# Kernel tuning notes

Hardware: AMD Instinct MI355X
Metric: run time of the kernel (lower is better)

The kernel has to match this reference:

```python
import jax, jax.numpy as jnp
import numpy as np

B, V, C, K = 8, 5000, 256, 200
LAMBDA_MIN, LAMBDA_MAX = 10.0, 1000.0


def get_mask(evals_x, evals_y, resolvant_gamma):
    # evals_[xy]: [B, K]
    scaling = jnp.maximum(jnp.max(evals_x, axis=1), jnp.max(evals_y, axis=1))[:, None]
    ex = (evals_x / scaling) ** resolvant_gamma  # [B, K]
    ey = (evals_y / scaling) ** resolvant_gamma  # [B, K]
    g1 = ex[:, :, None]  # [B, K, 1]
    g2 = ey[:, None, :]  # [B, 1, K]
    d1 = 1.0 / (g1 * g1 + 1.0)
    d2 = 1.0 / (g2 * g2 + 1.0)
    M_re = g2 * d2 - g1 * d1
    M_im = d2 - d1
    return M_re * M_re + M_im * M_im  # [B, K, K]


def setup_inputs() -> dict:
    key = jax.random.key(0)
    ks = jax.random.split(key, 6)
    feat_x = jax.random.normal(ks[0], (B, V, C), dtype=jnp.float32)
    feat_y = jax.random.normal(ks[1], (B, V, C), dtype=jnp.float32)
    # Laplacian-like nonnegative eigenvalues, bounded away from 0 so pow(., gamma) is smooth
    evals_x = jax.random.uniform(ks[2], (B, K), dtype=jnp.float32) * 10.0 + 0.01
    evals_y = jax.random.uniform(ks[3], (B, K), dtype=jnp.float32) * 10.0 + 0.01
    evecs_trans_x = jax.random.normal(ks[4], (B, K, V), dtype=jnp.float32) / np.sqrt(V)
    evecs_trans_y = jax.random.normal(ks[5], (B, K, V), dtype=jnp.float32) / np.sqrt(V)
    gamma_raw = jnp.asarray(0.0, dtype=jnp.float32)
    # softplus^{-1}(100) ~= 100 (log(exp(100)-1)); computed stably (exp(100) overflows fp32)
    lambda_raw = jnp.asarray(100.0, dtype=jnp.float32)
    return {
        "feat_x": feat_x, "feat_y": feat_y,
        "evals_x": evals_x, "evals_y": evals_y,
        "evecs_trans_x": evecs_trans_x, "evecs_trans_y": evecs_trans_y,
        "gamma_raw": gamma_raw, "lambda_raw": lambda_raw,
    }


def reference(feat_x, feat_y, evals_x, evals_y, evecs_trans_x, evecs_trans_y, gamma_raw, lambda_raw):
    # constrained parameters
    gamma = jax.nn.sigmoid(gamma_raw)
    lmbda = LAMBDA_MIN + jax.nn.softplus(lambda_raw) * (LAMBDA_MAX - LAMBDA_MIN) / LAMBDA_MAX
    lmbda = jnp.clip(lmbda, LAMBDA_MIN, LAMBDA_MAX)

    A = jnp.einsum('bkv,bvc->bkc', evecs_trans_x, feat_x)   # [B, K, C]
    Bc = jnp.einsum('bkv,bvc->bkc', evecs_trans_y, feat_y)  # [B, K, C]
    D = get_mask(evals_x, evals_y, gamma)                   # [B, K, K]

    A_A_t = jnp.einsum('bkc,blc->bkl', A, A)   # [B, K, K]
    B_A_t = jnp.einsum('bkc,blc->bkl', Bc, A)  # [B, K, K]

    # one batched solve for all (b, i): M[b,i] = A A^T + lmbda * diag(D[b,i,:])
    eye = jnp.eye(A_A_t.shape[-1], dtype=A_A_t.dtype)
    M = A_A_t[:, None, :, :] + lmbda * D[:, :, :, None] * eye  # [B, K, K, K]
    # Cxy[b, i, :] solves M[b,i] x = B_A_t[b, i, :]
    Cxy = jnp.linalg.solve(M, B_A_t[..., None])[..., 0]  # [B, K, K]
    return Cxy
```

## Files before the change

### kernel.cpp

```cpp
#include <hip/hip_runtime.h>
#include <math.h>

#define Bn 8
#define Vn 5000
#define Cn 256
#define Kn 200

#define AB_OFF  0
#define AAT_OFF 819200

__global__ __launch_bounds__(256) void k_gemm_ab(
    const float* __restrict__ fx, const float* __restrict__ fy,
    const float* __restrict__ etx, const float* __restrict__ ety,
    float* __restrict__ AB)
{
    __shared__ float Es[64 * 33];
    __shared__ float Fs[32 * 64];
    const int bid  = blockIdx.x;
    const int ks   = bid & 7;
    const int t    = bid >> 3;
    const int mat  = t >> 4;
    const int tile = t & 15;
    const int tr = tile >> 2, tc = tile & 3;
    const int b = mat & 7, which = mat >> 3;
    const float* __restrict__ E = (which ? ety : etx) + b * Kn * Vn;
    const float* __restrict__ F = (which ? fy : fx) + b * Vn * Cn;
    float* __restrict__ out = AB + mat * Kn * Cn;
    const int row0 = tr * 64, col0 = tc * 64;
    const int kstart = ks * 640;
    const int kend = (kstart + 640 < Vn) ? (kstart + 640) : Vn;
    const int tid = threadIdx.x;
    const int tx = tid & 15, ty = tid >> 4;
    float acc[4][4] = {};

    for (int k0 = kstart; k0 < kend; k0 += 32) {
#pragma unroll
        for (int i = 0; i < 8; ++i) {
            int idx = tid + i * 256;
            int r = idx >> 5, kk = idx & 31;
            int gr = row0 + r, gk = k0 + kk;
            Es[r * 33 + kk] = (gr < Kn && gk < kend) ? E[gr * Vn + gk] : 0.f;
        }
#pragma unroll
        for (int i = 0; i < 8; ++i) {
            int idx = tid + i * 256;
            int v = idx >> 6, cc = idx & 63;
            int gv = k0 + v;
            Fs[v * 64 + cc] = (gv < kend) ? F[gv * Cn + col0 + cc] : 0.f;
        }
        __syncthreads();
#pragma unroll
        for (int kk = 0; kk < 32; ++kk) {
            float a0 = Es[(ty * 4 + 0) * 33 + kk];
            float a1 = Es[(ty * 4 + 1) * 33 + kk];
            float a2 = Es[(ty * 4 + 2) * 33 + kk];
            float a3 = Es[(ty * 4 + 3) * 33 + kk];
            float4 bv = *(const float4*)&Fs[kk * 64 + tx * 4];
            acc[0][0] += a0 * bv.x; acc[0][1] += a0 * bv.y; acc[0][2] += a0 * bv.z; acc[0][3] += a0 * bv.w;
            acc[1][0] += a1 * bv.x; acc[1][1] += a1 * bv.y; acc[1][2] += a1 * bv.z; acc[1][3] += a1 * bv.w;
            acc[2][0] += a2 * bv.x; acc[2][1] += a2 * bv.y; acc[2][2] += a2 * bv.z; acc[2][3] += a2 * bv.w;
            acc[3][0] += a3 * bv.x; acc[3][1] += a3 * bv.y; acc[3][2] += a3 * bv.z; acc[3][3] += a3 * bv.w;
        }
        __syncthreads();
    }
#pragma unroll
    for (int m = 0; m < 4; ++m) {
        int gr = row0 + ty * 4 + m;
        if (gr < Kn) {
#pragma unroll
            for (int n = 0; n < 4; ++n)
                atomicAdd(&out[gr * Cn + col0 + tx * 4 + n], acc[m][n]);
        }
    }
}

__global__ __launch_bounds__(256) void k_gemm_nt(
    const float* __restrict__ AB, float* __restrict__ AAT)
{
    __shared__ float Xs[64 * 33];
    __shared__ float As[64 * 33];
    const int bid = blockIdx.x;
    const int mat = bid >> 4;
    const int tile = bid & 15;
    const int tr = tile >> 2, tc = tile & 3;
    const float* __restrict__ X  = AB + mat * Kn * Cn;
    const float* __restrict__ A2 = AB + (mat & 7) * Kn * Cn;
    float* __restrict__ out = AAT + mat * Kn * Kn;
    const int r0 = tr * 64, j0 = tc * 64;
    const int tid = threadIdx.x;
    const int tx = tid & 15, ty = tid >> 4;
    float acc[4][4] = {};

    for (int c0 = 0; c0 < Cn; c0 += 32) {
#pragma unroll
        for (int i = 0; i < 8; ++i) {
            int idx = tid + i * 256;
            int r = idx >> 5, kk = idx & 31;
            int gr = r0 + r;
            Xs[r * 33 + kk] = (gr < Kn) ? X[gr * Cn + c0 + kk] : 0.f;
            int gj = j0 + r;
            As[r * 33 + kk] = (gj < Kn) ? A2[gj * Cn + c0 + kk] : 0.f;
        }
        __syncthreads();
#pragma unroll
        for (int kk = 0; kk < 32; ++kk) {
            float a0 = Xs[(ty * 4 + 0) * 33 + kk];
            float a1 = Xs[(ty * 4 + 1) * 33 + kk];
            float a2 = Xs[(ty * 4 + 2) * 33 + kk];
            float a3 = Xs[(ty * 4 + 3) * 33 + kk];
            float b0 = As[(tx * 4 + 0) * 33 + kk];
            float b1 = As[(tx * 4 + 1) * 33 + kk];
            float b2 = As[(tx * 4 + 2) * 33 + kk];
            float b3 = As[(tx * 4 + 3) * 33 + kk];
            acc[0][0] += a0 * b0; acc[0][1] += a0 * b1; acc[0][2] += a0 * b2; acc[0][3] += a0 * b3;
            acc[1][0] += a1 * b0; acc[1][1] += a1 * b1; acc[1][2] += a1 * b2; acc[1][3] += a1 * b3;
            acc[2][0] += a2 * b0; acc[2][1] += a2 * b1; acc[2][2] += a2 * b2; acc[2][3] += a2 * b3;
            acc[3][0] += a3 * b0; acc[3][1] += a3 * b1; acc[3][2] += a3 * b2; acc[3][3] += a3 * b3;
        }
        __syncthreads();
    }
#pragma unroll
    for (int m = 0; m < 4; ++m) {
        int gr = r0 + ty * 4 + m;
        if (gr < Kn) {
#pragma unroll
            for (int n = 0; n < 4; ++n) {
                int gj = j0 + tx * 4 + n;
                if (gj < Kn) out[gr * Kn + gj] = acc[m][n];
            }
        }
    }
}

template<int QQ>
__device__ __forceinline__ void back_range(float y[4], const float* sM,
                                           const float* sInv, int lane,
                                           int khi, int klo)
{
    for (int k = khi; k >= klo; --k) {
        float xk = __shfl(y[QQ], k & 63) * sInv[k];
        if (lane == (k & 63)) y[QQ] = xk;
#pragma unroll
        for (int q2 = 0; q2 <= QQ; ++q2) {
            int r = lane + 64 * q2;
            if (r < k) y[q2] -= sM[r * 201 + k] * xk;
        }
    }
}

__global__ __launch_bounds__(512) void k_solve(
    const float* __restrict__ AAT,
    const float* __restrict__ evalx, const float* __restrict__ evaly,
    const float* __restrict__ graw, const float* __restrict__ lraw,
    float* __restrict__ out)
{
    __shared__ float sM[Kn * 201];
    __shared__ float sInv[Kn];
    __shared__ float sAux[8];
    const int bid = blockIdx.x;
    const int b = bid / 200;
    const int i = bid - b * 200;
    const int tid = threadIdx.x;
    const float* __restrict__ Sb = AAT + b * 40000;
    const float* __restrict__ Rb = AAT + 320000 + bid * 200;
    const float* __restrict__ ex = evalx + b * Kn;
    const float* __restrict__ ey = evaly + b * Kn;

    for (int e = tid; e < 40000; e += 512) {
        int r = e / 200;
        int c = e - r * 200;
        sM[r * 201 + c] = Sb[e];
    }
    if (tid < 200) sM[tid * 201 + 200] = Rb[tid];

    if (tid < 64) {
        float mx = 0.f;
        for (int j = tid; j < 200; j += 64) mx = fmaxf(mx, fmaxf(ex[j], ey[j]));
#pragma unroll
        for (int s = 32; s > 0; s >>= 1) mx = fmaxf(mx, __shfl_down(mx, s));
        if (tid == 0) sAux[0] = mx;
    }
    __syncthreads();

    if (tid < 200) {
        int r = tid;
        float s = sAux[0];
        float g = 1.f / (1.f + expf(-graw[0]));
        float lr = lraw[0];
        float sp = fmaxf(lr, 0.f) + log1pf(expf(-fabsf(lr)));
        float lmb = 10.f + sp * (990.f / 1000.f);
        lmb = fminf(fmaxf(lmb, 10.f), 1000.f);
        float gx = powf(ex[i] / s, g);
        float gy = powf(ey[r] / s, g);
        float d1 = 1.f / (gx * gx + 1.f);
        float d2 = 1.f / (gy * gy + 1.f);
        float re = gy * d2 - gx * d1;
        float im = d2 - d1;
        sM[r * 201 + r] += lmb * (re * re + im * im);
    }
    __syncthreads();

    const int w = tid >> 6, l = tid & 63;

    for (int k = 0; k < 200; k += 8) {
        if (tid < 64) {
            float p[4][8];
#pragma unroll
            for (int q = 0; q < 4; ++q) {
                int r = k + l + 64 * q;
                if (r < 200) {
#pragma unroll
                    for (int c = 0; c < 8; ++c) p[q][c] = sM[r * 201 + k + c];
                } else {
#pragma unroll
                    for (int c = 0; c < 8; ++c) p[q][c] = 0.f;
                }
            }
#pragma unroll
            for (int c = 0; c < 8; ++c) {
                float pivc = __shfl(p[0][c], c);
                float invp = 1.0f / pivc;
                float pr[8];
#pragma unroll
                for (int j = c + 1; j < 8; ++j) pr[j] = __shfl(p[0][j], c);
#pragma unroll
                for (int q = 0; q < 4; ++q) {
                    int r = k + l + 64 * q;
                    bool act = (r < 200) && (q > 0 || l > c);
                    if (act) {
                        float f = p[q][c] * invp;
                        p[q][c] = f;
#pragma unroll
                        for (int j = c + 1; j < 8; ++j) p[q][j] -= f * pr[j];
                    }
                }
            }
#pragma unroll
            for (int q = 0; q < 4; ++q) {
                int r = k + l + 64 * q;
                if (r < 200) {
#pragma unroll
                    for (int c = 0; c < 8; ++c) sM[r * 201 + k + c] = p[q][c];
                }
            }
        }
        __syncthreads();

        {
            int j = k + 8 + tid;
            if (j <= 200) {
                float u[8];
#pragma unroll
                for (int c = 0; c < 8; ++c) u[c] = sM[(k + c) * 201 + j];
#pragma unroll
                for (int c = 1; c < 8; ++c) {
                    float a = u[c];
#pragma unroll
                    for (int c2 = 0; c2 < c; ++c2)
                        a -= sM[(k + c) * 201 + k + c2] * u[c2];
                    u[c] = a;
                }
#pragma unroll
                for (int c = 0; c < 8; ++c) sM[(k + c) * 201 + j] = u[c];
            }
        }
        __syncthreads();

        {
            const int jb0 = k + 8;
            float pv[4][8];
#pragma unroll
            for (int ch = 0; ch < 4; ++ch) {
                int j = jb0 + ch * 64 + l;
                if (j <= 200) {
#pragma unroll
                    for (int c = 0; c < 8; ++c) pv[ch][c] = sM[(k + c) * 201 + j];
                }
            }
            for (int r = k + 8 + w; r < 200; r += 8) {
                float f[8];
#pragma unroll
                for (int c = 0; c < 8; ++c) f[c] = sM[r * 201 + k + c];
#pragma unroll
                for (int ch = 0; ch < 4; ++ch) {
                    int j = jb0 + ch * 64 + l;
                    if (j <= 200) {
                        float a = sM[r * 201 + j];
#pragma unroll
                        for (int c = 0; c < 8; ++c) a -= f[c] * pv[ch][c];
                        sM[r * 201 + j] = a;
                    }
                }
            }
        }
        __syncthreads();
    }

    if (tid < 200) sInv[tid] = 1.0f / sM[tid * 201 + tid];
    __syncthreads();

    if (tid < 64) {
        float y[4];
#pragma unroll
        for (int q = 0; q < 4; ++q) {
            int r = tid + 64 * q;
            y[q] = (r < 200) ? sM[r * 201 + 200] : 0.f;
        }
        back_range<3>(y, sM, sInv, tid, 199, 192);
        back_range<2>(y, sM, sInv, tid, 191, 128);
        back_range<1>(y, sM, sInv, tid, 127, 64);
        back_range<0>(y, sM, sInv, tid, 63, 0);
#pragma unroll
        for (int q = 0; q < 4; ++q) {
            int r = tid + 64 * q;
            if (r < 200) out[bid * 200 + r] = y[q];
        }
    }
}

extern "C" void kernel_launch(void* const* d_in, const int* in_sizes, int n_in,
                              void* d_out, int out_size, void* d_ws, size_t ws_size,
                              hipStream_t stream)
{
    const float* fx   = (const float*)d_in[0];
    const float* fy   = (const float*)d_in[1];
    const float* evx  = (const float*)d_in[2];
    const float* evy  = (const float*)d_in[3];
    const float* etx  = (const float*)d_in[4];
    const float* ety  = (const float*)d_in[5];
    const float* graw = (const float*)d_in[6];
    const float* lraw = (const float*)d_in[7];
    float* out = (float*)d_out;
    float* ws  = (float*)d_ws;

    hipMemsetAsync(ws + AB_OFF, 0, (size_t)16 * Kn * Cn * sizeof(float), stream);

    k_gemm_ab<<<dim3(2048), dim3(256), 0, stream>>>(fx, fy, etx, ety, ws + AB_OFF);
    k_gemm_nt<<<dim3(256), dim3(256), 0, stream>>>(ws + AB_OFF, ws + AAT_OFF);
    k_solve<<<dim3(1600), dim3(512), 0, stream>>>(ws + AAT_OFF, evx, evy, graw, lraw, out);
}
```

Before: 1.521 ms.

## Retile GEMMs with float4 loads and widen LU panel to 16 in solver

The first GEMM moves to 128x128 tiles with 8x8 register blocking, transposed shared staging and float4 global loads, using 16-way split-K. The NT GEMM gets a transposed shared layout so the inner loop reads float4. The per-(b,i) LU solver drops the padded 201 stride for a 200 stride with float4 accesses, widens the panel from 8 to 16 columns, and keeps the RHS in a separate buffer. It also adds a tail factorization for the last 8 rows and a blocked back substitution. The aim is fewer LDS transactions and barriers, at the cost of more registers and occupancy risk in the solver.

Measured after the change: 1.622 ms. 6.6% more time.

```diff
diff --git a/kernel.cpp b/kernel.cpp
--- a/kernel.cpp
+++ b/kernel.cpp
@@ -9,67 +9,79 @@
 #define AB_OFF  0
 #define AAT_OFF 819200
 
-__global__ __launch_bounds__(256) void k_gemm_ab(
+__global__ __launch_bounds__(256, 4) void k_gemm_ab(
     const float* __restrict__ fx, const float* __restrict__ fy,
     const float* __restrict__ etx, const float* __restrict__ ety,
     float* __restrict__ AB)
 {
-    __shared__ float Es[64 * 33];
-    __shared__ float Fs[32 * 64];
+    __shared__ __align__(16) float Es[16 * 132];
+    __shared__ __align__(16) float Fs[16 * 132];
     const int bid  = blockIdx.x;
-    const int ks   = bid & 7;
-    const int t    = bid >> 3;
-    const int mat  = t >> 4;
-    const int tile = t & 15;
-    const int tr = tile >> 2, tc = tile & 3;
+    const int ks   = bid & 15;
+    const int t    = bid >> 4;
+    const int mat  = t >> 2;
+    const int tile = t & 3;
+    const int row0 = (tile >> 1) * 128;
+    const int col0 = (tile & 1) * 128;
     const int b = mat & 7, which = mat >> 3;
     const float* __restrict__ E = (which ? ety : etx) + b * Kn * Vn;
     const float* __restrict__ F = (which ? fy : fx) + b * Vn * Cn;
     float* __restrict__ out = AB + mat * Kn * Cn;
-    const int row0 = tr * 64, col0 = tc * 64;
-    const int kstart = ks * 640;
-    const int kend = (kstart + 640 < Vn) ? (kstart + 640) : Vn;
+    const int kstart = ks * 320;
+    const int kend = (kstart + 320 < Vn) ? (kstart + 320) : Vn;
     const int tid = threadIdx.x;
     const int tx = tid & 15, ty = tid >> 4;
-    float acc[4][4] = {};
-
-    for (int k0 = kstart; k0 < kend; k0 += 32) {
-#pragma unroll
-        for (int i = 0; i < 8; ++i) {
-            int idx = tid + i * 256;
-            int r = idx >> 5, kk = idx & 31;
-            int gr = row0 + r, gk = k0 + kk;
-            Es[r * 33 + kk] = (gr < Kn && gk < kend) ? E[gr * Vn + gk] : 0.f;
-        }
-#pragma unroll
-        for (int i = 0; i < 8; ++i) {
-            int idx = tid + i * 256;
-            int v = idx >> 6, cc = idx & 63;
-            int gv = k0 + v;
-            Fs[v * 64 + cc] = (gv < kend) ? F[gv * Cn + col0 + cc] : 0.f;
-        }
-        __syncthreads();
-#pragma unroll
-        for (int kk = 0; kk < 32; ++kk) {
-            float a0 = Es[(ty * 4 + 0) * 33 + kk];
-            float a1 = Es[(ty * 4 + 1) * 33 + kk];
-            float a2 = Es[(ty * 4 + 2) * 33 + kk];
-            float a3 = Es[(ty * 4 + 3) * 33 + kk];
-            float4 bv = *(const float4*)&Fs[kk * 64 + tx * 4];
-            acc[0][0] += a0 * bv.x; acc[0][1] += a0 * bv.y; acc[0][2] += a0 * bv.z; acc[0][3] += a0 * bv.w;
-            acc[1][0] += a1 * bv.x; acc[1][1] += a1 * bv.y; acc[1][2] += a1 * bv.z; acc[1][3] += a1 * bv.w;
-            acc[2][0] += a2 * bv.x; acc[2][1] += a2 * bv.y; acc[2][2] += a2 * bv.z; acc[2][3] += a2 * bv.w;
-            acc[3][0] += a3 * bv.x; acc[3][1] += a3 * bv.y; acc[3][2] += a3 * bv.z; acc[3][3] += a3 * bv.w;
-        }
-        __syncthreads();
-    }
-#pragma unroll
-    for (int m = 0; m < 4; ++m) {
-        int gr = row0 + ty * 4 + m;
+    float acc[8][8] = {};
+
+    for (int k0 = kstart; k0 < kend; k0 += 16) {
+#pragma unroll
+        for (int i = 0; i < 2; ++i) {
+            int id = tid + i * 256;
+            int row = id >> 2;
+            int kq = (id & 3) << 2;
+            int gr = row0 + row;
+            float4 v = make_float4(0.f, 0.f, 0.f, 0.f);
+            if (gr < Kn && k0 + kq < kend)
+                v = *(const float4*)&E[gr * Vn + k0 + kq];
+            Es[(kq + 0) * 132 + row] = v.x;
+            Es[(kq + 1) * 132 + row] = v.y;
+            Es[(kq + 2) * 132 + row] = v.z;
+            Es[(kq + 3) * 132 + row] = v.w;
+        }
+#pragma unroll
+        for (int i = 0; i < 2; ++i) {
+            int id = tid + i * 256;
+            int v = id >> 5;
+            int cq = (id & 31) << 2;
+            float4 wv = make_float4(0.f, 0.f, 0.f, 0.f);
+            if (k0 + v < kend)
+                wv = *(const float4*)&F[(k0 + v) * Cn + col0 + cq];
+            *(float4*)&Fs[v * 132 + cq] = wv;
+        }
+        __syncthreads();
+#pragma unroll
+        for (int kk = 0; kk < 16; ++kk) {
+            float4 a0 = *(const float4*)&Es[kk * 132 + ty * 8];
+            float4 a1 = *(const float4*)&Es[kk * 132 + ty * 8 + 4];
+            float4 b0 = *(const float4*)&Fs[kk * 132 + tx * 8];
+            float4 b1 = *(const float4*)&Fs[kk * 132 + tx * 8 + 4];
+            float av[8] = {a0.x,a0.y,a0.z,a0.w,a1.x,a1.y,a1.z,a1.w};
+            float bv[8] = {b0.x,b0.y,b0.z,b0.w,b1.x,b1.y,b1.z,b1.w};
+#pragma unroll
+            for (int m = 0; m < 8; ++m)
+#pragma unroll
+                for (int n = 0; n < 8; ++n)
+                    acc[m][n] += av[m] * bv[n];
+        }
+        __syncthreads();
+    }
+#pragma unroll
+    for (int m = 0; m < 8; ++m) {
+        int gr = row0 + ty * 8 + m;
         if (gr < Kn) {
 #pragma unroll
-            for (int n = 0; n < 4; ++n)
-                atomicAdd(&out[gr * Cn + col0 + tx * 4 + n], acc[m][n]);
+            for (int n = 0; n < 8; ++n)
+                atomicAdd(&out[gr * Cn + col0 + tx * 8 + n], acc[m][n]);
         }
     }
 }
@@ -77,8 +89,8 @@
 __global__ __launch_bounds__(256) void k_gemm_nt(
     const float* __restrict__ AB, float* __restrict__ AAT)
 {
-    __shared__ float Xs[64 * 33];
-    __shared__ float As[64 * 33];
+    __shared__ __align__(16) float Xs[32 * 68];
+    __shared__ __align__(16) float As[32 * 68];
     const int bid = blockIdx.x;
     const int mat = bid >> 4;
     const int tile = bid & 15;
@@ -93,29 +105,37 @@
 
     for (int c0 = 0; c0 < Cn; c0 += 32) {
 #pragma unroll
-        for (int i = 0; i < 8; ++i) {
-            int idx = tid + i * 256;
-            int r = idx >> 5, kk = idx & 31;
-            int gr = r0 + r;
-            Xs[r * 33 + kk] = (gr < Kn) ? X[gr * Cn + c0 + kk] : 0.f;
-            int gj = j0 + r;
-            As[r * 33 + kk] = (gj < Kn) ? A2[gj * Cn + c0 + kk] : 0.f;
+        for (int i = 0; i < 2; ++i) {
+            int id = tid + i * 256;
+            int row = id >> 3;
+            int kq = (id & 7) << 2;
+            int gr = r0 + row;
+            float4 v = (gr < Kn) ? *(const float4*)&X[gr * Cn + c0 + kq]
+                                 : make_float4(0.f, 0.f, 0.f, 0.f);
+            Xs[(kq + 0) * 68 + row] = v.x;
+            Xs[(kq + 1) * 68 + row] = v.y;
+            Xs[(kq + 2) * 68 + row] = v.z;
+            Xs[(kq + 3) * 68 + row] = v.w;
+            int gj = j0 + row;
+            float4 u = (gj < Kn) ? *(const float4*)&A2[gj * Cn + c0 + kq]
+                                 : make_float4(0.f, 0.f, 0.f, 0.f);
+            As[(kq + 0) * 68 + row] = u.x;
+            As[(kq + 1) * 68 + row] = u.y;
+            As[(kq + 2) * 68 + row] = u.z;
+            As[(kq + 3) * 68 + row] = u.w;
         }
         __syncthreads();
 #pragma unroll
         for (int kk = 0; kk < 32; ++kk) {
-            float a0 = Xs[(ty * 4 + 0) * 33 + kk];
-            float a1 = Xs[(ty * 4 + 1) * 33 + kk];
-            float a2 = Xs[(ty * 4 + 2) * 33 + kk];
-            float a3 = Xs[(ty * 4 + 3) * 33 + kk];
-            float b0 = As[(tx * 4 + 0) * 33 + kk];
-            float b1 = As[(tx * 4 + 1) * 33 + kk];
-            float b2 = As[(tx * 4 + 2) * 33 + kk];
-            float b3 = As[(tx * 4 + 3) * 33 + kk];
-            acc[0][0] += a0 * b0; acc[0][1] += a0 * b1; acc[0][2] += a0 * b2; acc[0][3] += a0 * b3;
-            acc[1][0] += a1 * b0; acc[1][1] += a1 * b1; acc[1][2] += a1 * b2; acc[1][3] += a1 * b3;
-            acc[2][0] += a2 * b0; acc[2][1] += a2 * b1; acc[2][2] += a2 * b2; acc[2][3] += a2 * b3;
-            acc[3][0] += a3 * b0; acc[3][1] += a3 * b1; acc[3][2] += a3 * b2; acc[3][3] += a3 * b3;
+            float4 a = *(const float4*)&Xs[kk * 68 + ty * 4];
+            float4 bb = *(const float4*)&As[kk * 68 + tx * 4];
+            float av[4] = {a.x, a.y, a.z, a.w};
+            float bv[4] = {bb.x, bb.y, bb.z, bb.w};
+#pragma unroll
+            for (int m = 0; m < 4; ++m)
+#pragma unroll
+                for (int n = 0; n < 4; ++n)
+                    acc[m][n] += av[m] * bv[n];
         }
         __syncthreads();
     }
@@ -132,57 +152,44 @@
     }
 }
 
-template<int QQ>
-__device__ __forceinline__ void back_range(float y[4], const float* sM,
-                                           const float* sInv, int lane,
-                                           int khi, int klo)
-{
-    for (int k = khi; k >= klo; --k) {
-        float xk = __shfl(y[QQ], k & 63) * sInv[k];
-        if (lane == (k & 63)) y[QQ] = xk;
-#pragma unroll
-        for (int q2 = 0; q2 <= QQ; ++q2) {
-            int r = lane + 64 * q2;
-            if (r < k) y[q2] -= sM[r * 201 + k] * xk;
-        }
-    }
-}
-
-__global__ __launch_bounds__(512) void k_solve(
+__global__ __launch_bounds__(512, 2) void k_solve(
     const float* __restrict__ AAT,
     const float* __restrict__ evalx, const float* __restrict__ evaly,
     const float* __restrict__ graw, const float* __restrict__ lraw,
     float* __restrict__ out)
 {
-    __shared__ float sM[Kn * 201];
-    __shared__ float sInv[Kn];
+    __shared__ __align__(16) float sM[Kn * 200];
+    __shared__ __align__(16) float sR4[Kn * 4];
+    __shared__ __align__(16) float sUr4[16 * 4];
     __shared__ float sAux[8];
     const int bid = blockIdx.x;
     const int b = bid / 200;
+    const int tid = threadIdx.x;
     const int i = bid - b * 200;
-    const int tid = threadIdx.x;
     const float* __restrict__ Sb = AAT + b * 40000;
     const float* __restrict__ Rb = AAT + 320000 + bid * 200;
     const float* __restrict__ ex = evalx + b * Kn;
     const float* __restrict__ ey = evaly + b * Kn;
-
-    for (int e = tid; e < 40000; e += 512) {
-        int r = e / 200;
-        int c = e - r * 200;
-        sM[r * 201 + c] = Sb[e];
-    }
-    if (tid < 200) sM[tid * 201 + 200] = Rb[tid];
+    const int w = tid >> 6, l = tid & 63;
+
+    {
+        const float4* Sb4 = (const float4*)Sb;
+        float4* sM4 = (float4*)sM;
+        for (int e = tid; e < 10000; e += 512) sM4[e] = Sb4[e];
+    }
+    if (tid < Kn) *(float4*)&sR4[tid * 4] = make_float4(Rb[tid], 0.f, 0.f, 0.f);
+    if (tid < 64) sUr4[tid] = 0.f;
 
     if (tid < 64) {
         float mx = 0.f;
-        for (int j = tid; j < 200; j += 64) mx = fmaxf(mx, fmaxf(ex[j], ey[j]));
+        for (int j2 = tid; j2 < Kn; j2 += 64) mx = fmaxf(mx, fmaxf(ex[j2], ey[j2]));
 #pragma unroll
         for (int s = 32; s > 0; s >>= 1) mx = fmaxf(mx, __shfl_down(mx, s));
         if (tid == 0) sAux[0] = mx;
     }
     __syncthreads();
 
-    if (tid < 200) {
+    if (tid < Kn) {
         int r = tid;
         float s = sAux[0];
         float g = 1.f / (1.f + expf(-graw[0]));
@@ -196,124 +203,216 @@
         float d2 = 1.f / (gy * gy + 1.f);
         float re = gy * d2 - gx * d1;
         float im = d2 - d1;
-        sM[r * 201 + r] += lmb * (re * re + im * im);
+        sM[r * 200 + r] += lmb * (re * re + im * im);
     }
     __syncthreads();
 
-    const int w = tid >> 6, l = tid & 63;
-
-    for (int k = 0; k < 200; k += 8) {
+    for (int k = 0; k < 192; k += 16) {
+        const int jb0 = k + 16;
+
         if (tid < 64) {
-            float p[4][8];
+            float p[4][16];
 #pragma unroll
             for (int q = 0; q < 4; ++q) {
                 int r = k + l + 64 * q;
-                if (r < 200) {
-#pragma unroll
-                    for (int c = 0; c < 8; ++c) p[q][c] = sM[r * 201 + k + c];
+                if (r < Kn) {
+#pragma unroll
+                    for (int jq = 0; jq < 4; ++jq) {
+                        float4 v = *(const float4*)&sM[r * 200 + k + jq * 4];
+                        p[q][jq * 4 + 0] = v.x; p[q][jq * 4 + 1] = v.y;
+                        p[q][jq * 4 + 2] = v.z; p[q][jq * 4 + 3] = v.w;
+                    }
                 } else {
 #pragma unroll
-                    for (int c = 0; c < 8; ++c) p[q][c] = 0.f;
-                }
-            }
-#pragma unroll
-            for (int c = 0; c < 8; ++c) {
+                    for (int j2 = 0; j2 < 16; ++j2) p[q][j2] = 0.f;
+                }
+            }
+#pragma unroll
+            for (int c = 0; c < 16; ++c) {
                 float pivc = __shfl(p[0][c], c);
                 float invp = 1.0f / pivc;
-                float pr[8];
-#pragma unroll
-                for (int j = c + 1; j < 8; ++j) pr[j] = __shfl(p[0][j], c);
+                float pr[16];
+#pragma unroll
+                for (int j2 = 0; j2 < 16; ++j2)
+                    if (j2 > c) pr[j2] = __shfl(p[0][j2], c);
 #pragma unroll
                 for (int q = 0; q < 4; ++q) {
                     int r = k + l + 64 * q;
-                    bool act = (r < 200) && (q > 0 || l > c);
+                    bool act = (r < Kn) && (q > 0 || l > c);
                     if (act) {
                         float f = p[q][c] * invp;
                         p[q][c] = f;
 #pragma unroll
-                        for (int j = c + 1; j < 8; ++j) p[q][j] -= f * pr[j];
+                        for (int j2 = 0; j2 < 16; ++j2)
+                            if (j2 > c) p[q][j2] -= f * pr[j2];
                     }
                 }
             }
 #pragma unroll
             for (int q = 0; q < 4; ++q) {
                 int r = k + l + 64 * q;
-                if (r < 200) {
-#pragma unroll
-                    for (int c = 0; c < 8; ++c) sM[r * 201 + k + c] = p[q][c];
+                if (r < Kn) {
+#pragma unroll
+                    for (int jq = 0; jq < 4; ++jq) {
+                        *(float4*)&sM[r * 200 + k + jq * 4] =
+                            make_float4(p[q][jq * 4 + 0], p[q][jq * 4 + 1],
+                                        p[q][jq * 4 + 2], p[q][jq * 4 + 3]);
+                    }
                 }
             }
         }
         __syncthreads();
 
         {
-            int j = k + 8 + tid;
-            if (j <= 200) {
-                float u[8];
-#pragma unroll
-                for (int c = 0; c < 8; ++c) u[c] = sM[(k + c) * 201 + j];
-#pragma unroll
-                for (int c = 1; c < 8; ++c) {
+            const int nt = 184 - k;
+            if (tid <= nt) {
+                const bool rhs = (tid == nt);
+                const int j = jb0 + tid;
+                float u[16];
+                if (!rhs) {
+#pragma unroll
+                    for (int c = 0; c < 16; ++c) u[c] = sM[(k + c) * 200 + j];
+                } else {
+#pragma unroll
+                    for (int c = 0; c < 16; ++c) u[c] = sR4[(k + c) * 4];
+                }
+#pragma unroll
+                for (int c = 1; c < 16; ++c) {
+                    float4 Lr[4];
+#pragma unroll
+                    for (int mq = 0; mq < 4; ++mq)
+                        if (mq * 4 < c)
+                            Lr[mq] = *(const float4*)&sM[(k + c) * 200 + k + mq * 4];
                     float a = u[c];
 #pragma unroll
-                    for (int c2 = 0; c2 < c; ++c2)
-                        a -= sM[(k + c) * 201 + k + c2] * u[c2];
+                    for (int c2 = 0; c2 < 16; ++c2)
+                        if (c2 < c) a -= ((const float*)Lr)[c2] * u[c2];
                     u[c] = a;
                 }
-#pragma unroll
-                for (int c = 0; c < 8; ++c) sM[(k + c) * 201 + j] = u[c];
+                if (!rhs) {
+#pragma unroll
+                    for (int c = 0; c < 16; ++c) sM[(k + c) * 200 + j] = u[c];
+                } else {
+#pragma unroll
+                    for (int c = 0; c < 16; ++c) {
+                        sR4[(k + c) * 4] = u[c];
+                        sUr4[c * 4] = u[c];
+                    }
+                }
             }
         }
         __syncthreads();
 
         {
-            const int jb0 = k + 8;
-            float pv[4][8];
-#pragma unroll
-            for (int ch = 0; ch < 4; ++ch) {
-                int j = jb0 + ch * 64 + l;
-                if (j <= 200) {
-#pragma unroll
-                    for (int c = 0; c < 8; ++c) pv[ch][c] = sM[(k + c) * 201 + j];
-                }
-            }
-            for (int r = k + 8 + w; r < 200; r += 8) {
-                float f[8];
-#pragma unroll
-                for (int c = 0; c < 8; ++c) f[c] = sM[r * 201 + k + c];
-#pragma unroll
-                for (int ch = 0; ch < 4; ++ch) {
-                    int j = jb0 + ch * 64 + l;
-                    if (j <= 200) {
-                        float a = sM[r * 201 + j];
-#pragma unroll
-                        for (int c = 0; c < 8; ++c) a -= f[c] * pv[ch][c];
-                        sM[r * 201 + j] = a;
+            const int nl = (184 - k) >> 2;
+            if (l <= nl) {
+                const bool rhs = (l == nl);
+                const float* pvbase = rhs ? sUr4 : &sM[k * 200 + jb0 + 4 * l];
+                const int pvstride = rhs ? 4 : 200;
+                float4 pv[16];
+#pragma unroll
+                for (int c = 0; c < 16; ++c)
+                    pv[c] = *(const float4*)&pvbase[c * pvstride];
+                float* crow = rhs ? sR4 : &sM[jb0 + 4 * l];
+                const int cstride = rhs ? 4 : 200;
+                for (int r = jb0 + w; r < Kn; r += 8) {
+                    const float* fr = &sM[r * 200 + k];
+                    float4 f0 = *(const float4*)&fr[0];
+                    float4 f1 = *(const float4*)&fr[4];
+                    float4 f2 = *(const float4*)&fr[8];
+                    float4 f3 = *(const float4*)&fr[12];
+                    float fv[16] = {f0.x,f0.y,f0.z,f0.w, f1.x,f1.y,f1.z,f1.w,
+                                    f2.x,f2.y,f2.z,f2.w, f3.x,f3.y,f3.z,f3.w};
+                    float4 cv = *(const float4*)&crow[r * cstride];
+#pragma unroll
+                    for (int c = 0; c < 16; ++c) {
+                        cv.x -= fv[c] * pv[c].x;
+                        cv.y -= fv[c] * pv[c].y;
+                        cv.z -= fv[c] * pv[c].z;
+                        cv.w -= fv[c] * pv[c].w;
                     }
-                }
-            }
-        }
-        __syncthreads();
-    }
-
-    if (tid < 200) sInv[tid] = 1.0f / sM[tid * 201 + tid];
+                    *(float4*)&crow[r * cstride] = cv;
+                }
+            }
+        }
+        __syncthreads();
+    }
+
+    if (tid < 64) {
+        float e[9];
+        const int r = 192 + l;
+        const bool act = (l < 8);
+        if (act) {
+            float4 t0 = *(const float4*)&sM[r * 200 + 192];
+            float4 t1 = *(const float4*)&sM[r * 200 + 196];
+            e[0] = t0.x; e[1] = t0.y; e[2] = t0.z; e[3] = t0.w;
+            e[4] = t1.x; e[5] = t1.y; e[6] = t1.z; e[7] = t1.w;
+            e[8] = sR4[r * 4];
+        } else {
+#pragma unroll
+            for (int j2 = 0; j2 < 9; ++j2) e[j2] = 0.f;
+        }
+#pragma unroll
+        for (int c = 0; c < 8; ++c) {
+            float pive = __shfl(e[c], c);
+            float invp = 1.0f / pive;
+            float pr[9];
+#pragma unroll
+            for (int j2 = 0; j2 < 9; ++j2)
+                if (j2 > c) pr[j2] = __shfl(e[j2], c);
+            if (act && l > c) {
+                float f = e[c] * invp;
+#pragma unroll
+                for (int j2 = 0; j2 < 9; ++j2)
+                    if (j2 > c) e[j2] -= f * pr[j2];
+            }
+        }
+        if (act) {
+            *(float4*)&sM[r * 200 + 192] = make_float4(e[0], e[1], e[2], e[3]);
+            *(float4*)&sM[r * 200 + 196] = make_float4(e[4], e[5], e[6], e[7]);
+            sR4[r * 4] = e[8];
+        }
+    }
     __syncthreads();
 
     if (tid < 64) {
         float y[4];
 #pragma unroll
         for (int q = 0; q < 4; ++q) {
-            int r = tid + 64 * q;
-            y[q] = (r < 200) ? sM[r * 201 + 200] : 0.f;
-        }
-        back_range<3>(y, sM, sInv, tid, 199, 192);
-        back_range<2>(y, sM, sInv, tid, 191, 128);
-        back_range<1>(y, sM, sInv, tid, 127, 64);
-        back_range<0>(y, sM, sInv, tid, 63, 0);
+            int r = l + 64 * q;
+            y[q] = (r < Kn) ? sR4[r * 4] : 0.f;
+        }
+        for (int kb = 196; kb >= 0; kb -= 4) {
+            float4 cv[4];
+#pragma unroll
+            for (int q = 0; q < 4; ++q) {
+                int r = l + 64 * q;
+                cv[q] = (r < Kn) ? *(const float4*)&sM[r * 200 + kb]
+                                 : make_float4(0.f, 0.f, 0.f, 0.f);
+            }
+#pragma unroll
+            for (int c = 3; c >= 0; --c) {
+                const int kk2 = kb + c;
+                const int src = kk2 & 63;
+                float xl = 0.f;
+#pragma unroll
+                for (int q = 0; q < 4; ++q) {
+                    int r = l + 64 * q;
+                    if (r == kk2) xl = y[q] / ((const float*)&cv[q])[c];
+                }
+                float xk = __shfl(xl, src);
+#pragma unroll
+                for (int q = 0; q < 4; ++q) {
+                    int r = l + 64 * q;
+                    if (r == kk2) y[q] = xk;
+                    else if (r < kk2) y[q] -= ((const float*)&cv[q])[c] * xk;
+                }
+            }
+        }
 #pragma unroll
         for (int q = 0; q < 4; ++q) {
-            int r = tid + 64 * q;
-            if (r < 200) out[bid * 200 + r] = y[q];
+            int r = l + 64 * q;
+            if (r < Kn) out[bid * 200 + r] = y[q];
         }
     }
 }
@@ -335,7 +434,7 @@
 
     hipMemsetAsync(ws + AB_OFF, 0, (size_t)16 * Kn * Cn * sizeof(float), stream);
 
-    k_gemm_ab<<<dim3(2048), dim3(256), 0, stream>>>(fx, fy, etx, ety, ws + AB_OFF);
+    k_gemm_ab<<<dim3(1024), dim3(256), 0, stream>>>(fx, fy, etx, ety, ws + AB_OFF);
     k_gemm_nt<<<dim3(256), dim3(256), 0, stream>>>(ws + AB_OFF, ws + AAT_OFF);
     k_solve<<<dim3(1600), dim3(512), 0, stream>>>(ws + AAT_OFF, evx, evy, graw, lraw, out);
 }
```
